# Optimization experiments

Hardware: AMD Instinct MI355X
Metric: run time of the kernel (lower is better)

## Reference

```python
import itertools
import jax, jax.numpy as jnp
import numpy as np

B, N, ETA, K, Z, HID, NATOM, NBOND = 128, 40, 64, 32, 32, 256, 24, 5
A = B * N
E = B * (N * (N - 1) // 2)
TAU = 1.0  # gumbel_softmax_temperature default


def _bn(x, g, b, eps=1e-5):
    # BatchNorm1d in training mode: batch statistics, biased variance
    m = jnp.mean(x, axis=0)
    v = jnp.var(x, axis=0)
    return (x - m) * jax.lax.rsqrt(v + eps) * g + b


def _prelu(x, a):
    return jnp.where(x >= 0, x, a * x)


def _mlp(x, w1, b1, g, be, a, w2, b2):
    # Linear -> BatchNorm1d -> PReLU -> Linear
    return _prelu(_bn(x @ w1 + b1, g, be), a) @ w2 + b2


def setup_inputs() -> dict:
    key = jax.random.key(0)
    ks = jax.random.split(key, 16)
    # static all-pairs edge index per graph, offset per graph (mirrors decode_z)
    pairs = np.array(list(itertools.combinations(range(N), 2)), dtype=np.int64)  # [P,2]
    offs = (np.arange(B, dtype=np.int64) * N)[:, None, None]
    edge_index = jnp.asarray((pairs[None] + offs).reshape(-1, 2))  # [E,2]
    node_graph_idx = jnp.asarray(np.repeat(np.arange(B, dtype=np.int64), N))  # [A]

    def w(k, shape, fan_in):
        return jax.random.normal(k, shape, jnp.float32) / np.sqrt(fan_in).astype(np.float32)

    return {
        "eta": jax.random.normal(ks[0], (B, ETA), jnp.float32),
        "gumbel_u": jax.random.uniform(ks[1], (A, K), jnp.float32, 1e-6, 1.0 - 1e-6),
        "noise_z": jax.random.normal(ks[2], (A, Z), jnp.float32),
        "edge_index": edge_index,
        "node_graph_idx": node_graph_idx,
        # cluster_mlp
        "cw1": w(ks[3], (ETA, HID), ETA), "cb1": jnp.zeros(HID), "cg": jnp.ones(HID), "cbe": jnp.zeros(HID), "ca": jnp.float32(0.25),
        "cw2": w(ks[4], (HID, K), HID), "cb2": jnp.zeros(K),
        # mixture params (torch: randn means, zero log-sigmas)
        "cm": jax.random.normal(ks[5], (K, Z), jnp.float32), "cls": jnp.zeros((K, Z), jnp.float32),
        # atom_classifier
        "aw1": w(ks[6], (Z, HID), Z), "ab1": jnp.zeros(HID), "ag": jnp.ones(HID), "abe": jnp.zeros(HID), "aa": jnp.float32(0.25),
        "aw2": w(ks[7], (HID, NATOM), HID), "ab2": jnp.zeros(NATOM),
        # bond bilinear tensor [d, a, b]
        "bm": jax.random.normal(ks[8], (Z, Z, Z), jnp.float32) / np.sqrt(Z).astype(np.float32),
        # bond_type_mlp
        "bw1": w(ks[9], (Z, HID), Z), "bb1": jnp.zeros(HID), "bg": jnp.ones(HID), "bbe": jnp.zeros(HID), "ba": jnp.float32(0.25),
        "bw2": w(ks[10], (HID, NBOND), HID), "bb2": jnp.zeros(NBOND),
    }


def reference(eta, gumbel_u, noise_z, edge_index, node_graph_idx,
              cw1, cb1, cg, cbe, ca, cw2, cb2, cm, cls,
              aw1, ab1, ag, abe, aa, aw2, ab2,
              bm, bw1, bb1, bg, bbe, ba, bw2, bb2):
    # decode_eta: pi = softmax(cluster_mlp(eta)); log_pi = log(pi)
    log_pi = jax.nn.log_softmax(_mlp(eta, cw1, cb1, cg, cbe, ca, cw2, cb2), axis=1)
    # repeat_interleave(log_pi, num_atoms) -> per-atom logits
    logits = log_pi[node_graph_idx]  # [A, K]
    # gumbel_softmax hard=True (straight-through)
    g = -jnp.log(-jnp.log(gumbel_u))
    y_soft = jax.nn.softmax((logits + g) / TAU, axis=1)
    y_hard = jax.nn.one_hot(jnp.argmax(y_soft, axis=1), K, dtype=y_soft.dtype)
    c = y_hard - jax.lax.stop_gradient(y_soft) + y_soft  # [A, K]
    # select cluster mean / log-sigma, reparameterize
    mu = c @ cm                 # [A, Z]
    log_sigma = c @ cls         # [A, Z]
    z = noise_z * jnp.exp(jnp.clip(log_sigma, -20.0, 30.0)) + mu
    # decode_z
    atom_types = _mlp(z, aw1, ab1, ag, abe, aa, aw2, ab2)  # [A, NATOM]
    Wm = 0.5 * (bm + jnp.swapaxes(bm, 1, 2))  # symmetrize over (a, b)
    zi = z[edge_index[:, 0]]  # [E, Z]
    zj = z[edge_index[:, 1]]  # [E, Z]
    t = jnp.einsum('ea,dab->edb', zi, Wm)       # [E, Z, Z]
    edge_feat = jnp.einsum('edb,eb->ed', t, zj)  # z_i^T W_d z_j, [E, Z]
    edge_types = jax.nn.softmax(_mlp(edge_feat, bw1, bb1, bg, bbe, ba, bw2, bb2), axis=1)  # [E, NBOND]
    return atom_types, edge_types
```

## Files before the change

### kernel.cpp

```cpp
#include <hip/hip_runtime.h>
#include <math.h>

#define BG    128
#define NN    40
#define AK    32
#define ZD    32
#define HIDN  256
#define ETAD  64
#define NATOM 24
#define NBOND 5
#define NA    (BG*NN)
#define EPG   (NN*(NN-1)/2)
#define NE    (BG*EPG)

typedef __attribute__((ext_vector_type(8))) short bf16x8;
typedef __attribute__((ext_vector_type(4))) float f32x4;

__device__ __forceinline__ unsigned short f2bf(float f) {
    union { float f; unsigned int u; } x; x.f = f;
    unsigned int r = x.u + 0x7fffu + ((x.u >> 16) & 1u);
    return (unsigned short)(r >> 16);
}
__device__ __forceinline__ unsigned int pk2bf(float lo, float hi) {
    return (unsigned int)f2bf(lo) | ((unsigned int)f2bf(hi) << 16);
}

__global__ __launch_bounds__(256) void k_pre(const float* __restrict__ bm,
                                             const float* __restrict__ bw1,
                                             const float* __restrict__ aw1,
                                             const float* __restrict__ aw2,
                                             const float* __restrict__ eta,
                                             const float* __restrict__ cw1,
                                             const float* __restrict__ cb1,
                                             unsigned short* __restrict__ wmpk,
                                             unsigned short* __restrict__ bpack,
                                             unsigned short* __restrict__ apk1,
                                             unsigned short* __restrict__ apk2,
                                             float* __restrict__ h1,
                                             float* __restrict__ cpart,
                                             float* __restrict__ zacc) {
    int b = blockIdx.x, t = threadIdx.x;
    if (b < 128) {
        int idx = b*256 + t;
        int d = idx >> 10;
        int Bt = (idx >> 9) & 1, ln = (idx >> 3) & 63, j = idx & 7;
        int al = Bt*16 + (ln & 15);
        int be = (ln >> 4)*8 + j;
        float v = 0.5f * (bm[d*1024 + al*32 + be] + bm[d*1024 + be*32 + al]);
        wmpk[idx] = f2bf(v);
    } else if (b < 160) {
        int idx = (b - 128)*256 + t;
        int ct = idx >> 9, rem = idx & 511;
        int lane = rem >> 3, j = rem & 7;
        bpack[idx] = f2bf(bw1[((lane >> 4)*8 + j)*HIDN + ct*16 + (lane & 15)]);
    } else if (b < 192) {
        int idx = (b - 160)*256 + t;
        int ct = idx >> 9, rem = idx & 511;
        int lane = rem >> 3, j = rem & 7;
        apk1[idx] = f2bf(aw1[((lane >> 4)*8 + j)*HIDN + ct*16 + (lane & 15)]);
    } else if (b < 224) {
        int idx = (b - 192)*256 + t;
        int f = idx >> 9, rem = idx & 511;
        int lane = rem >> 3, j = rem & 7;
        int kc = f >> 1, ot = f & 1;
        int col = ot*16 + (lane & 15);
        int k = kc*32 + (lane >> 4)*8 + j;
        apk2[idx] = (col < NATOM) ? f2bf(aw2[k*NATOM + col]) : 0;
    } else if (b < 232) {
        __shared__ float es[16*ETAD];
        int b2 = b - 224;
        int r0 = b2*16;
        for (int i = t; i < 16*ETAD; i += 256) es[i] = eta[r0*ETAD + i];
        __syncthreads();
        int c = t;
        float bias = cb1[c], s = 0.f, ss = 0.f;
        for (int r = 0; r < 16; ++r) {
            float acc = bias;
#pragma unroll
            for (int a = 0; a < ETAD; ++a) acc += es[r*ETAD + a] * cw1[a*HIDN + c];
            h1[(r0 + r)*HIDN + c] = acc;
            s += acc; ss += acc*acc;
        }
        cpart[b2*512 + c] = s;
        cpart[b2*512 + 256 + c] = ss;
    } else {
        for (int i = t; i < 2112; i += 256) zacc[i] = 0.f;
    }
}

__global__ __launch_bounds__(256) void k_edge_class(const float* __restrict__ h1,
                                                    const float* __restrict__ cpart,
                                                    const float* __restrict__ cg,
                                                    const float* __restrict__ cbe,
                                                    const float* __restrict__ ca,
                                                    const float* __restrict__ cw2,
                                                    const float* __restrict__ cb2,
                                                    const float* __restrict__ gum,
                                                    const float* __restrict__ noise,
                                                    const float* __restrict__ cm,
                                                    const float* __restrict__ cls,
                                                    const unsigned short* __restrict__ wmpk,
                                                    float* __restrict__ z,
                                                    float* __restrict__ mom_z,
                                                    float* __restrict__ ef) {
    __shared__ float zl[NN*36];
    __shared__ float p[HIDN];
    __shared__ float vp2[256];
    __shared__ float oo[AK];
    __shared__ float lp[AK];
    __shared__ unsigned short zfrag[3*512];
    __shared__ unsigned short Tf[4][3*512];
    __shared__ float efl[EPG*9];
    int t = threadIdx.x;
    int g = blockIdx.x >> 2, dg = blockIdx.x & 3;
    float aP = ca[0];

    {
        float s = 0.f, ss = 0.f;
#pragma unroll
        for (int q = 0; q < 8; ++q) { s += cpart[q*512 + t]; ss += cpart[q*512 + 256 + t]; }
        float m = s * (1.0f/(float)BG);
        float v = ss * (1.0f/(float)BG) - m*m;
        float x = h1[g*HIDN + t];
        float xn = (x - m) * (1.0f/sqrtf(v + 1e-5f)) * cg[t] + cbe[t];
        p[t] = xn >= 0.f ? xn : aP*xn;
    }
    __syncthreads();
    {
        int k = t & 31, part = t >> 5;
        float acc = 0.f;
        const float* pc = &p[part*32];
        const float* wc = &cw2[(part*32)*AK + k];
#pragma unroll
        for (int c = 0; c < 32; ++c) acc += pc[c] * wc[c*AK];
        vp2[t] = acc;
    }
    __syncthreads();
    if (t < AK) {
        float acc = cb2[t];
#pragma unroll
        for (int q = 0; q < 8; ++q) acc += vp2[q*32 + t];
        oo[t] = acc;
    }
    __syncthreads();
    if (t < AK) {
        float m = -INFINITY;
#pragma unroll
        for (int k = 0; k < AK; ++k) m = fmaxf(m, oo[k]);
        float S = 0.f;
#pragma unroll
        for (int k = 0; k < AK; ++k) S += expf(oo[k] - m);
        lp[t] = oo[t] - m - logf(S);
    }
    __syncthreads();
    {
        int lane = t & 31;
#pragma unroll
        for (int nb = 0; nb < 5; ++nb) {
            int node = nb*8 + (t >> 5);
            int n = g*NN + node;
            float u = gum[(size_t)n*AK + lane];
            float x = lp[lane] - logf(-logf(u));
            float m = x;
#pragma unroll
            for (int s = 1; s < 32; s <<= 1) m = fmaxf(m, __shfl_xor(m, s, 32));
            float e = expf(x - m);
            float S = e;
#pragma unroll
            for (int s = 1; s < 32; s <<= 1) S += __shfl_xor(S, s, 32);
            unsigned long long bal = __ballot(x == m);
            unsigned grp = (unsigned)(bal >> (t & 32));
            int am = __ffs(grp) - 1;
            float best = 1.0f / S;
            float cam = (1.0f - best) + best;
            float ls = cam * cls[am*ZD + lane];
            ls = fminf(fmaxf(ls, -20.0f), 30.0f);
            float zv = noise[(size_t)n*ZD + lane]*expf(ls) + cam*cm[am*ZD + lane];
            zl[node*36 + lane] = zv;
            if (dg == 0) z[(size_t)n*ZD + lane] = zv;
        }
    }
    __syncthreads();
    if (dg == 0) {
        int a = t >> 3, b4 = (t & 7) << 2;
        float ax = 0.f, ay = 0.f, az = 0.f, aw = 0.f;
        float mx = 0.f, my = 0.f, mz = 0.f, mw = 0.f;
        for (int r = 0; r < NN; ++r) {
            float  va = zl[r*36 + a];
            float4 vb = *(const float4*)&zl[r*36 + b4];
            ax += va*vb.x; ay += va*vb.y; az += va*vb.z; aw += va*vb.w;
            mx += vb.x;    my += vb.y;    mz += vb.z;    mw += vb.w;
        }
        atomicAdd(&mom_z[a*ZD + b4 + 0], ax);
        atomicAdd(&mom_z[a*ZD + b4 + 1], ay);
        atomicAdd(&mom_z[a*ZD + b4 + 2], az);
        atomicAdd(&mom_z[a*ZD + b4 + 3], aw);
        if (a == 0) {
            atomicAdd(&mom_z[ZD*ZD + b4 + 0], mx);
            atomicAdd(&mom_z[ZD*ZD + b4 + 1], my);
            atomicAdd(&mom_z[ZD*ZD + b4 + 2], mz);
            atomicAdd(&mom_z[ZD*ZD + b4 + 3], mw);
        }
    }
    if (t < 192) {
        int I = t >> 6, ln = t & 63;
        int row = I*16 + (ln & 15), c0 = (ln >> 4)*8;
        unsigned int pk[4] = {0u, 0u, 0u, 0u};
        if (row < NN) {
            float4 v0 = *(const float4*)&zl[row*36 + c0];
            float4 v1 = *(const float4*)&zl[row*36 + c0 + 4];
            pk[0] = pk2bf(v0.x, v0.y); pk[1] = pk2bf(v0.z, v0.w);
            pk[2] = pk2bf(v1.x, v1.y); pk[3] = pk2bf(v1.z, v1.w);
        }
        *(uint4*)&zfrag[(I*64 + ln)*8] = make_uint4(pk[0], pk[1], pk[2], pk[3]);
    }
    __syncthreads();

    int w = t >> 6, lane = t & 63;
    int l15 = lane & 15, gq = lane >> 4;
    f32x4 zero4 = {0.f, 0.f, 0.f, 0.f};

    bf16x8 zf[3];
#pragma unroll
    for (int I = 0; I < 3; ++I) zf[I] = *(const bf16x8*)&zfrag[I*512 + lane*8];

    for (int dk = 0; dk < 2; ++dk) {
        int dd = w*2 + dk;
        int d  = dg*8 + dd;
        bf16x8 wA[2];
        wA[0] = *(const bf16x8*)&wmpk[(d*2 + 0)*512 + lane*8];
        wA[1] = *(const bf16x8*)&wmpk[(d*2 + 1)*512 + lane*8];

        unsigned short* tw = &Tf[w][0];
        int gqp_lo = (gq >> 1);
        int jo     = (gq & 1)*4;
#pragma unroll
        for (int Bt = 0; Bt < 2; ++Bt) {
#pragma unroll
            for (int I = 0; I < 3; ++I) {
                f32x4 c = __builtin_amdgcn_mfma_f32_16x16x32_bf16(wA[Bt], zf[I], zero4, 0, 0, 0);
                int gqp = Bt*2 + gqp_lo;
                int pos = I*512 + gqp*128 + l15*8 + jo;
                unsigned int d0 = pk2bf(c[0], c[1]);
                unsigned int d1 = pk2bf(c[2], c[3]);
                *(uint2*)&tw[pos] = make_uint2(d0, d1);
            }
        }
        __syncthreads();

        bf16x8 tf[3];
#pragma unroll
        for (int J = 0; J < 3; ++J) tf[J] = *(const bf16x8*)&Tf[w][J*512 + lane*8];

#pragma unroll
        for (int I = 0; I < 3; ++I) {
#pragma unroll
            for (int J = I; J < 3; ++J) {
                f32x4 gacc = __builtin_amdgcn_mfma_f32_16x16x32_bf16(zf[I], tf[J], zero4, 0, 0, 0);
                int j = J*16 + l15;
                if (j < NN) {
#pragma unroll
                    for (int r = 0; r < 4; ++r) {
                        int i = I*16 + 4*gq + r;
                        if (i < j) {
                            int e = i*(79 - i)/2 + (j - i - 1);
                            efl[e*9 + dd] = gacc[r];
                        }
                    }
                }
            }
        }
        __syncthreads();
    }

    size_t gE = (size_t)g * EPG;
    for (int idx = t; idx < EPG*8; idx += 256) {
        int e = idx >> 3, dd = idx & 7;
        ef[(gE + e)*ZD + dg*8 + dd] = efl[e*9 + dd];
    }
}

#define MOMB 192
__global__ __launch_bounds__(256) void k_moment(const float* __restrict__ src,
                                                float* __restrict__ mom, int nchunks) {
    __shared__ float sm[ZD*ZD + ZD];
    int t = threadIdx.x;
    for (int i = t; i < ZD*ZD + ZD; i += 256) sm[i] = 0.f;
    __syncthreads();
    int lane = t & 63, wv = t >> 6;
    int l15 = lane & 15, g4 = lane >> 4;
    int wgid = blockIdx.x * 4 + wv;
    const int nw = MOMB * 4;
    f32x4 aII = {0,0,0,0}, aIJ = {0,0,0,0}, aJI = {0,0,0,0}, aJJ = {0,0,0,0};
    float mI = 0.f, mJ = 0.f;
    for (int ch = wgid; ch < nchunks; ch += nw) {
        const float* p = src + ((size_t)ch*32 + g4*8)*ZD + l15;
        float vI[8], vJ[8];
#pragma unroll
        for (int j = 0; j < 8; ++j) { vI[j] = p[j*ZD]; vJ[j] = p[j*ZD + 16]; }
        bf16x8 fI, fJ;
#pragma unroll
        for (int j = 0; j < 8; ++j) {
            fI[j] = (short)f2bf(vI[j]); fJ[j] = (short)f2bf(vJ[j]);
            mI += vI[j]; mJ += vJ[j];
        }
        aII = __builtin_amdgcn_mfma_f32_16x16x32_bf16(fI, fI, aII, 0, 0, 0);
        aIJ = __builtin_amdgcn_mfma_f32_16x16x32_bf16(fI, fJ, aIJ, 0, 0, 0);
        aJI = __builtin_amdgcn_mfma_f32_16x16x32_bf16(fJ, fI, aJI, 0, 0, 0);
        aJJ = __builtin_amdgcn_mfma_f32_16x16x32_bf16(fJ, fJ, aJJ, 0, 0, 0);
    }
#pragma unroll
    for (int r = 0; r < 4; ++r) {
        int row = g4*4 + r;
        atomicAdd(&sm[row*ZD + l15],             aII[r]);
        atomicAdd(&sm[row*ZD + 16 + l15],        aIJ[r]);
        atomicAdd(&sm[(16 + row)*ZD + l15],      aJI[r]);
        atomicAdd(&sm[(16 + row)*ZD + 16 + l15], aJJ[r]);
    }
    atomicAdd(&sm[ZD*ZD + l15], mI);
    atomicAdd(&sm[ZD*ZD + 16 + l15], mJ);
    __syncthreads();
    for (int i = t; i < ZD*ZD + ZD; i += 256) atomicAdd(&mom[i], sm[i]);
}

__global__ __launch_bounds__(256) void k_prep2(const float* __restrict__ mom_z,
                                               const float* __restrict__ mom_ef,
                                               const float* __restrict__ aw1,
                                               const float* __restrict__ ab1,
                                               const float* __restrict__ ag,
                                               const float* __restrict__ abe,
                                               const float* __restrict__ bw1,
                                               const float* __restrict__ bb1,
                                               const float* __restrict__ bg,
                                               const float* __restrict__ bbe,
                                               float* __restrict__ ascale,
                                               float* __restrict__ ashift,
                                               float* __restrict__ bscale,
                                               float* __restrict__ bshift) {
    bool bond = blockIdx.x >= 8;
    const float* mom = bond ? mom_ef : mom_z;
    const float* w1  = bond ? bw1 : aw1;
    const float* b1  = bond ? bb1 : ab1;
    const float* g   = bond ? bg  : ag;
    const float* be  = bond ? bbe : abe;
    float inv_n      = bond ? (1.0f/(float)NE) : (1.0f/(float)NA);
    float* scale     = bond ? bscale : ascale;
    float* shift     = bond ? bshift : ashift;

    __shared__ float mean[ZD];
    __shared__ float cov[ZD*ZD];
    __shared__ float vp[256], mp[256];
    int t = threadIdx.x;
    if (t < ZD) mean[t] = mom[ZD*ZD + t] * inv_n;
    __syncthreads();
    for (int pp = t; pp < ZD*ZD; pp += 256) {
        int a = pp >> 5, b = pp & 31;
        cov[pp] = mom[pp] * inv_n - mean[a]*mean[b];
    }
    __syncthreads();
    int c = (blockIdx.x & 7) * 32 + (t & 31);
    int part = t >> 5;
    float wr[ZD];
#pragma unroll
    for (int b = 0; b < ZD; ++b) wr[b] = w1[b*HIDN + c];
    float var = 0.f, mh = 0.f;
#pragma unroll
    for (int q = 0; q < 4; ++q) {
        int a = part*4 + q;
        float tmp = 0.f;
#pragma unroll
        for (int b = 0; b < ZD; ++b) tmp += cov[a*ZD + b] * wr[b];
        var += tmp * wr[a];
        mh  += mean[a] * wr[a];
    }
    vp[t] = var; mp[t] = mh;
    __syncthreads();
    if (t < 32) {
        float v = 0.f, m = 0.f;
#pragma unroll
        for (int q = 0; q < 8; ++q) { v += vp[q*32 + t]; m += mp[q*32 + t]; }
        m += b1[c];
        float rs = rsqrtf(fmaxf(v, 0.f) + 1e-5f) * g[c];
        scale[c] = rs;
        shift[c] = be[c] - m * rs;
    }
}

#define PSH 264
#define ATOMB (NA/64)
#define BROWS4 128
__global__ __launch_bounds__(256) void k_out(const float* __restrict__ z,
                                             const unsigned short* __restrict__ apk1,
                                             const unsigned short* __restrict__ apk2,
                                             const float* __restrict__ ab1,
                                             const float* __restrict__ ascale,
                                             const float* __restrict__ ashift,
                                             const float* __restrict__ aa,
                                             const float* __restrict__ ab2,
                                             const float* __restrict__ ef,
                                             const unsigned short* __restrict__ bpack,
                                             const float* __restrict__ bb1,
                                             const float* __restrict__ bscale,
                                             const float* __restrict__ bshift,
                                             const float* __restrict__ ba,
                                             const float* __restrict__ bw2,
                                             const float* __restrict__ bb2,
                                             float* __restrict__ out_atom,
                                             float* __restrict__ out_bond) {
    __shared__ unsigned short smu[4*16*PSH];
    int t = threadIdx.x;
    int w = t >> 6, lane = t & 63;
    int l15 = lane & 15, gq = lane >> 4;
    f32x4 zero4 = {0.f, 0.f, 0.f, 0.f};

    if (blockIdx.x < ATOMB) {
        size_t r0 = (size_t)blockIdx.x * 64 + (size_t)w * 16;
        float aP = aa[0];
        unsigned short* ptw = &smu[w*16*PSH];

        const float* zp = &z[(r0 + l15)*ZD + gq*8];
        float4 z0 = *(const float4*)zp;
        float4 z1 = *(const float4*)(zp + 4);
        bf16x8 af;
        af[0] = (short)f2bf(z0.x); af[1] = (short)f2bf(z0.y);
        af[2] = (short)f2bf(z0.z); af[3] = (short)f2bf(z0.w);
        af[4] = (short)f2bf(z1.x); af[5] = (short)f2bf(z1.y);
        af[6] = (short)f2bf(z1.z); af[7] = (short)f2bf(z1.w);

#pragma unroll
        for (int ct = 0; ct < 16; ++ct) {
            bf16x8 bf = *(const bf16x8*)&apk1[ct*512 + lane*8];
            f32x4 c = __builtin_amdgcn_mfma_f32_16x16x32_bf16(af, bf, zero4, 0, 0, 0);
            int ch = ct*16 + l15;
            float sc = ascale[ch];
            float sh = ashift[ch] + ab1[ch]*sc;
#pragma unroll
            for (int r = 0; r < 4; ++r) {
                float xn = c[r]*sc + sh;
                float pv = xn >= 0.f ? xn : aP*xn;
                ptw[(4*gq + r)*PSH + ch] = f2bf(pv);
            }
        }

        f32x4 o0 = zero4, o1 = zero4;
#pragma unroll
        for (int kc = 0; kc < 8; ++kc) {
            bf16x8 af2 = *(const bf16x8*)&ptw[l15*PSH + kc*32 + gq*8];
            bf16x8 b0 = *(const bf16x8*)&apk2[(kc*2 + 0)*512 + lane*8];
            bf16x8 b1 = *(const bf16x8*)&apk2[(kc*2 + 1)*512 + lane*8];
            o0 = __builtin_amdgcn_mfma_f32_16x16x32_bf16(af2, b0, o0, 0, 0, 0);
            o1 = __builtin_amdgcn_mfma_f32_16x16x32_bf16(af2, b1, o1, 0, 0, 0);
        }
#pragma unroll
        for (int r = 0; r < 4; ++r) {
            size_t row = r0 + 4*gq + r;
            out_atom[row*NATOM + l15] = o0[r] + ab2[l15];
            if (l15 < 8) out_atom[row*NATOM + 16 + l15] = o1[r] + ab2[16 + l15];
        }
        return;
    }

    float* w2s = (float*)smu;
    float* scs = w2s + HIDN*NBOND;
    float* shs = scs + HIDN;
    size_t r0 = (size_t)(blockIdx.x - ATOMB) * BROWS4;

    for (int i = t; i < HIDN*NBOND; i += 256) w2s[i] = bw2[i];
    { float sc = bscale[t]; scs[t] = sc; shs[t] = bshift[t] + bb1[t]*sc; }
    __syncthreads();

    float aP = ba[0];
    float b2r[NBOND];
#pragma unroll
    for (int k = 0; k < NBOND; ++k) b2r[k] = bb2[k];

#pragma unroll
    for (int rt = 0; rt < 2; ++rt) {
        size_t rowt = r0 + (size_t)(w*2 + rt)*16;
        const float* ar = &ef[(rowt + l15)*ZD + gq*8];
        float4 a0 = *(const float4*)ar;
        float4 a1 = *(const float4*)(ar + 4);
        bf16x8 af;
        af[0] = (short)f2bf(a0.x); af[1] = (short)f2bf(a0.y);
        af[2] = (short)f2bf(a0.z); af[3] = (short)f2bf(a0.w);
        af[4] = (short)f2bf(a1.x); af[5] = (short)f2bf(a1.y);
        af[6] = (short)f2bf(a1.z); af[7] = (short)f2bf(a1.w);

        float part[4][NBOND];
#pragma unroll
        for (int r = 0; r < 4; ++r)
#pragma unroll
            for (int k = 0; k < NBOND; ++k) part[r][k] = 0.f;

#pragma unroll
        for (int h = 0; h < 2; ++h) {
            bf16x8 bfr[8];
#pragma unroll
            for (int q = 0; q < 8; ++q)
                bfr[q] = *(const bf16x8*)&bpack[(h*8 + q)*512 + lane*8];
            f32x4 acc[8];
#pragma unroll
            for (int q = 0; q < 8; ++q)
                acc[q] = __builtin_amdgcn_mfma_f32_16x16x32_bf16(af, bfr[q], zero4, 0, 0, 0);
#pragma unroll
            for (int q = 0; q < 8; ++q) {
                int c = (h*8 + q)*16 + l15;
                float sc = scs[c], sh = shs[c];
                float w0 = w2s[c*NBOND+0], w1v = w2s[c*NBOND+1], w2v = w2s[c*NBOND+2];
                float w3 = w2s[c*NBOND+3], w4 = w2s[c*NBOND+4];
#pragma unroll
                for (int r = 0; r < 4; ++r) {
                    float xn = acc[q][r]*sc + sh;
                    float pv = xn >= 0.f ? xn : aP*xn;
                    part[r][0] += pv*w0; part[r][1] += pv*w1v; part[r][2] += pv*w2v;
                    part[r][3] += pv*w3; part[r][4] += pv*w4;
                }
            }
        }

#pragma unroll
        for (int s = 1; s < 16; s <<= 1) {
#pragma unroll
            for (int r = 0; r < 4; ++r)
#pragma unroll
                for (int k = 0; k < NBOND; ++k)
                    part[r][k] += __shfl_xor(part[r][k], s, 64);
        }

        if (l15 == 0) {
#pragma unroll
            for (int r = 0; r < 4; ++r) {
                size_t row = rowt + gq*4 + r;
                float lg[NBOND];
                float m = -INFINITY;
#pragma unroll
                for (int k = 0; k < NBOND; ++k) { lg[k] = part[r][k] + b2r[k]; m = fmaxf(m, lg[k]); }
                float S = 0.f;
#pragma unroll
                for (int k = 0; k < NBOND; ++k) { lg[k] = expf(lg[k] - m); S += lg[k]; }
                float invS = 1.f / S;
#pragma unroll
                for (int k = 0; k < NBOND; ++k) out_bond[row*NBOND + k] = lg[k] * invS;
            }
        }
    }
}

extern "C" void kernel_launch(void* const* d_in, const int* in_sizes, int n_in,
                              void* d_out, int out_size, void* d_ws, size_t ws_size,
                              hipStream_t stream) {
    (void)in_sizes; (void)n_in; (void)out_size; (void)ws_size;
    const float* eta  = (const float*)d_in[0];
    const float* gum  = (const float*)d_in[1];
    const float* noi  = (const float*)d_in[2];
    const float* cw1  = (const float*)d_in[5];
    const float* cb1  = (const float*)d_in[6];
    const float* cgp  = (const float*)d_in[7];
    const float* cbe  = (const float*)d_in[8];
    const float* ca   = (const float*)d_in[9];
    const float* cw2  = (const float*)d_in[10];
    const float* cb2  = (const float*)d_in[11];
    const float* cm   = (const float*)d_in[12];
    const float* cls  = (const float*)d_in[13];
    const float* aw1  = (const float*)d_in[14];
    const float* ab1  = (const float*)d_in[15];
    const float* ag   = (const float*)d_in[16];
    const float* abe  = (const float*)d_in[17];
    const float* aa   = (const float*)d_in[18];
    const float* aw2  = (const float*)d_in[19];
    const float* ab2  = (const float*)d_in[20];
    const float* bm   = (const float*)d_in[21];
    const float* bw1  = (const float*)d_in[22];
    const float* bb1  = (const float*)d_in[23];
    const float* bg   = (const float*)d_in[24];
    const float* bbe  = (const float*)d_in[25];
    const float* ba   = (const float*)d_in[26];
    const float* bw2  = (const float*)d_in[27];
    const float* bb2  = (const float*)d_in[28];
    float* out = (float*)d_out;
    float* ws  = (float*)d_ws;

    float*          mom_z  = ws;
    float*          mom_ef = ws + 1056;
    float*          ascale = ws + 2112;
    float*          ashift = ws + 2368;
    float*          bscale = ws + 2624;
    float*          bshift = ws + 2880;
    float*          cpart  = ws + 3136;
    unsigned short* bpack  = (unsigned short*)(ws + 7232);
    unsigned short* apk1   = (unsigned short*)(ws + 11328);
    unsigned short* apk2   = (unsigned short*)(ws + 15424);
    unsigned short* wmpk   = (unsigned short*)(ws + 19520);
    float*          h1     = ws + 35904;
    float*          zbuf   = ws + 68672;
    float*          efb    = ws + 232512;

    k_pre       <<<dim3(233),      dim3(256), 0, stream>>>(bm, bw1, aw1, aw2, eta, cw1, cb1,
                                                           wmpk, bpack, apk1, apk2, h1, cpart, ws);
    k_edge_class<<<dim3(4*BG),     dim3(256), 0, stream>>>(h1, cpart, cgp, cbe, ca, cw2, cb2,
                                                           gum, noi, cm, cls, wmpk,
                                                           zbuf, mom_z, efb);
    k_moment    <<<dim3(MOMB),     dim3(256), 0, stream>>>(efb, mom_ef, NE/32);
    k_prep2     <<<dim3(16),       dim3(256), 0, stream>>>(mom_z, mom_ef, aw1, ab1, ag, abe,
                                                           bw1, bb1, bg, bbe,
                                                           ascale, ashift, bscale, bshift);
    k_out       <<<dim3(ATOMB + NE/BROWS4), dim3(256), 0, stream>>>(
                                                           zbuf, apk1, apk2, ab1, ascale, ashift,
                                                           aa, ab2,
                                                           efb, bpack, bb1, bscale, bshift,
                                                           ba, bw2, bb2,
                                                           out, out + NA*NATOM);
}
```

Before: 81.17 us.

## Remove BN-prep kernel by fusing stats into moment and output kernels

Deletes the separate k_prep2 launch. The atom BatchNorm scale/shift is now computed by an extra block of k_moment, and every bond block of k_out recomputes the bond scale/shift from the edge moments in its prologue. The edge-feature buffer also moves to a dim-group-major layout ([4][NE][8]), so the edge-kernel stores and the moment/output loads become contiguous. This saves one launch and its dependency gap, at the cost of redundant per-block covariance work in the many k_out bond blocks. The bond bias bb1 is dropped from the shift, which is exact because the batch mean cancels it.

```diff
diff --git a/kernel.cpp b/kernel.cpp
--- a/kernel.cpp
+++ b/kernel.cpp
@@ -273,18 +273,60 @@
         __syncthreads();
     }
 
-    size_t gE = (size_t)g * EPG;
+    size_t base = ((size_t)dg*NE + (size_t)g*EPG)*8;
     for (int idx = t; idx < EPG*8; idx += 256) {
         int e = idx >> 3, dd = idx & 7;
-        ef[(gE + e)*ZD + dg*8 + dd] = efl[e*9 + dd];
+        ef[base + idx] = efl[e*9 + dd];
     }
 }
 
 #define MOMB 192
 __global__ __launch_bounds__(256) void k_moment(const float* __restrict__ src,
-                                                float* __restrict__ mom, int nchunks) {
+                                                float* __restrict__ mom,
+                                                const float* __restrict__ mom_z,
+                                                const float* __restrict__ aw1,
+                                                const float* __restrict__ ab1,
+                                                const float* __restrict__ ag,
+                                                const float* __restrict__ abe,
+                                                float* __restrict__ ascale,
+                                                float* __restrict__ ashift,
+                                                int nchunks) {
     __shared__ float sm[ZD*ZD + ZD];
     int t = threadIdx.x;
+
+    if (blockIdx.x == MOMB) {
+        float* cov = sm;
+        float* mean = sm + ZD*ZD;
+        if (t < ZD) mean[t] = mom_z[ZD*ZD + t] * (1.0f/(float)NA);
+        __syncthreads();
+        for (int pp = t; pp < ZD*ZD; pp += 256) {
+            int a = pp >> 5, b = pp & 31;
+            cov[pp] = mom_z[pp] * (1.0f/(float)NA) - mean[a]*mean[b];
+        }
+        __syncthreads();
+        int c = t;
+        float wr[ZD];
+#pragma unroll
+        for (int b = 0; b < ZD; ++b) wr[b] = aw1[b*HIDN + c];
+        float var = 0.f, mh = 0.f;
+        for (int a = 0; a < ZD; ++a) {
+            float tmp = 0.f;
+            const float4* cr = (const float4*)&cov[a*ZD];
+#pragma unroll
+            for (int b4 = 0; b4 < 8; ++b4) {
+                float4 cv = cr[b4];
+                tmp += cv.x*wr[b4*4] + cv.y*wr[b4*4+1] + cv.z*wr[b4*4+2] + cv.w*wr[b4*4+3];
+            }
+            var += tmp * wr[a];
+            mh  += mean[a] * wr[a];
+        }
+        mh += ab1[c];
+        float rs = rsqrtf(fmaxf(var, 0.f) + 1e-5f) * ag[c];
+        ascale[c] = rs;
+        ashift[c] = abe[c] - mh * rs;
+        return;
+    }
+
     for (int i = t; i < ZD*ZD + ZD; i += 256) sm[i] = 0.f;
     __syncthreads();
     int lane = t & 63, wv = t >> 6;
@@ -293,11 +335,14 @@
     const int nw = MOMB * 4;
     f32x4 aII = {0,0,0,0}, aIJ = {0,0,0,0}, aJI = {0,0,0,0}, aJJ = {0,0,0,0};
     float mI = 0.f, mJ = 0.f;
+    int segI = l15 >> 3, offI = l15 & 7;
     for (int ch = wgid; ch < nchunks; ch += nw) {
-        const float* p = src + ((size_t)ch*32 + g4*8)*ZD + l15;
+        size_t br = (size_t)ch*32 + g4*8;
+        const float* pI = src + ((size_t)segI*NE + br)*8 + offI;
+        const float* pJ = src + ((size_t)(2 + segI)*NE + br)*8 + offI;
         float vI[8], vJ[8];
 #pragma unroll
-        for (int j = 0; j < 8; ++j) { vI[j] = p[j*ZD]; vJ[j] = p[j*ZD + 16]; }
+        for (int j = 0; j < 8; ++j) { vI[j] = pI[j*8]; vJ[j] = pJ[j*8]; }
         bf16x8 fI, fJ;
 #pragma unroll
         for (int j = 0; j < 8; ++j) {
@@ -321,69 +366,6 @@
     atomicAdd(&sm[ZD*ZD + 16 + l15], mJ);
     __syncthreads();
     for (int i = t; i < ZD*ZD + ZD; i += 256) atomicAdd(&mom[i], sm[i]);
-}
-
-__global__ __launch_bounds__(256) void k_prep2(const float* __restrict__ mom_z,
-                                               const float* __restrict__ mom_ef,
-                                               const float* __restrict__ aw1,
-                                               const float* __restrict__ ab1,
-                                               const float* __restrict__ ag,
-                                               const float* __restrict__ abe,
-                                               const float* __restrict__ bw1,
-                                               const float* __restrict__ bb1,
-                                               const float* __restrict__ bg,
-                                               const float* __restrict__ bbe,
-                                               float* __restrict__ ascale,
-                                               float* __restrict__ ashift,
-                                               float* __restrict__ bscale,
-                                               float* __restrict__ bshift) {
-    bool bond = blockIdx.x >= 8;
-    const float* mom = bond ? mom_ef : mom_z;
-    const float* w1  = bond ? bw1 : aw1;
-    const float* b1  = bond ? bb1 : ab1;
-    const float* g   = bond ? bg  : ag;
-    const float* be  = bond ? bbe : abe;
-    float inv_n      = bond ? (1.0f/(float)NE) : (1.0f/(float)NA);
-    float* scale     = bond ? bscale : ascale;
-    float* shift     = bond ? bshift : ashift;
-
-    __shared__ float mean[ZD];
-    __shared__ float cov[ZD*ZD];
-    __shared__ float vp[256], mp[256];
-    int t = threadIdx.x;
-    if (t < ZD) mean[t] = mom[ZD*ZD + t] * inv_n;
-    __syncthreads();
-    for (int pp = t; pp < ZD*ZD; pp += 256) {
-        int a = pp >> 5, b = pp & 31;
-        cov[pp] = mom[pp] * inv_n - mean[a]*mean[b];
-    }
-    __syncthreads();
-    int c = (blockIdx.x & 7) * 32 + (t & 31);
-    int part = t >> 5;
-    float wr[ZD];
-#pragma unroll
-    for (int b = 0; b < ZD; ++b) wr[b] = w1[b*HIDN + c];
-    float var = 0.f, mh = 0.f;
-#pragma unroll
-    for (int q = 0; q < 4; ++q) {
-        int a = part*4 + q;
-        float tmp = 0.f;
-#pragma unroll
-        for (int b = 0; b < ZD; ++b) tmp += cov[a*ZD + b] * wr[b];
-        var += tmp * wr[a];
-        mh  += mean[a] * wr[a];
-    }
-    vp[t] = var; mp[t] = mh;
-    __syncthreads();
-    if (t < 32) {
-        float v = 0.f, m = 0.f;
-#pragma unroll
-        for (int q = 0; q < 8; ++q) { v += vp[q*32 + t]; m += mp[q*32 + t]; }
-        m += b1[c];
-        float rs = rsqrtf(fmaxf(v, 0.f) + 1e-5f) * g[c];
-        scale[c] = rs;
-        shift[c] = be[c] - m * rs;
-    }
 }
 
 #define PSH 264
@@ -399,9 +381,10 @@
                                              const float* __restrict__ ab2,
                                              const float* __restrict__ ef,
                                              const unsigned short* __restrict__ bpack,
-                                             const float* __restrict__ bb1,
-                                             const float* __restrict__ bscale,
-                                             const float* __restrict__ bshift,
+                                             const float* __restrict__ mom_ef,
+                                             const float* __restrict__ bw1,
+                                             const float* __restrict__ bg,
+                                             const float* __restrict__ bbe,
                                              const float* __restrict__ ba,
                                              const float* __restrict__ bw2,
                                              const float* __restrict__ bb2,
@@ -460,13 +443,42 @@
         return;
     }
 
-    float* w2s = (float*)smu;
-    float* scs = w2s + HIDN*NBOND;
-    float* shs = scs + HIDN;
+    float* w2s  = (float*)smu;
+    float* scs  = w2s + HIDN*NBOND;
+    float* shs  = scs + HIDN;
+    float* mean = shs + HIDN;
+    float* cov  = mean + 32;
     size_t r0 = (size_t)(blockIdx.x - ATOMB) * BROWS4;
 
     for (int i = t; i < HIDN*NBOND; i += 256) w2s[i] = bw2[i];
-    { float sc = bscale[t]; scs[t] = sc; shs[t] = bshift[t] + bb1[t]*sc; }
+    if (t < ZD) mean[t] = mom_ef[ZD*ZD + t] * (1.0f/(float)NE);
+    __syncthreads();
+    for (int pp = t; pp < ZD*ZD; pp += 256) {
+        int a = pp >> 5, bb = pp & 31;
+        cov[pp] = mom_ef[pp] * (1.0f/(float)NE) - mean[a]*mean[bb];
+    }
+    __syncthreads();
+    {
+        int c = t;
+        float wr[ZD];
+#pragma unroll
+        for (int bb = 0; bb < ZD; ++bb) wr[bb] = bw1[bb*HIDN + c];
+        float var = 0.f, mh = 0.f;
+        for (int a = 0; a < ZD; ++a) {
+            float tmp = 0.f;
+            const float4* cr = (const float4*)&cov[a*ZD];
+#pragma unroll
+            for (int b4 = 0; b4 < 8; ++b4) {
+                float4 cv = cr[b4];
+                tmp += cv.x*wr[b4*4] + cv.y*wr[b4*4+1] + cv.z*wr[b4*4+2] + cv.w*wr[b4*4+3];
+            }
+            var += tmp * wr[a];
+            mh  += mean[a] * wr[a];
+        }
+        float rs = rsqrtf(fmaxf(var, 0.f) + 1e-5f) * bg[c];
+        scs[c] = rs;
+        shs[c] = bbe[c] - mh * rs;
+    }
     __syncthreads();
 
     float aP = ba[0];
@@ -477,7 +489,7 @@
 #pragma unroll
     for (int rt = 0; rt < 2; ++rt) {
         size_t rowt = r0 + (size_t)(w*2 + rt)*16;
-        const float* ar = &ef[(rowt + l15)*ZD + gq*8];
+        const float* ar = &ef[((size_t)gq*NE + rowt + l15)*8];
         float4 a0 = *(const float4*)ar;
         float4 a1 = *(const float4*)(ar + 4);
         bf16x8 af;
@@ -577,6 +589,7 @@
     const float* ba   = (const float*)d_in[26];
     const float* bw2  = (const float*)d_in[27];
     const float* bb2  = (const float*)d_in[28];
+    (void)bb1;
     float* out = (float*)d_out;
     float* ws  = (float*)d_ws;
 
@@ -584,30 +597,27 @@
     float*          mom_ef = ws + 1056;
     float*          ascale = ws + 2112;
     float*          ashift = ws + 2368;
-    float*          bscale = ws + 2624;
-    float*          bshift = ws + 2880;
-    float*          cpart  = ws + 3136;
-    unsigned short* bpack  = (unsigned short*)(ws + 7232);
-    unsigned short* apk1   = (unsigned short*)(ws + 11328);
-    unsigned short* apk2   = (unsigned short*)(ws + 15424);
-    unsigned short* wmpk   = (unsigned short*)(ws + 19520);
-    float*          h1     = ws + 35904;
-    float*          zbuf   = ws + 68672;
-    float*          efb    = ws + 232512;
+    float*          cpart  = ws + 2624;
+    unsigned short* bpack  = (unsigned short*)(ws + 6720);
+    unsigned short* apk1   = (unsigned short*)(ws + 10816);
+    unsigned short* apk2   = (unsigned short*)(ws + 14912);
+    unsigned short* wmpk   = (unsigned short*)(ws + 19008);
+    float*          h1     = ws + 35392;
+    float*          zbuf   = ws + 68160;
+    float*          efb    = ws + 232000;
 
     k_pre       <<<dim3(233),      dim3(256), 0, stream>>>(bm, bw1, aw1, aw2, eta, cw1, cb1,
                                                            wmpk, bpack, apk1, apk2, h1, cpart, ws);
     k_edge_class<<<dim3(4*BG),     dim3(256), 0, stream>>>(h1, cpart, cgp, cbe, ca, cw2, cb2,
                                                            gum, noi, cm, cls, wmpk,
                                                            zbuf, mom_z, efb);
-    k_moment    <<<dim3(MOMB),     dim3(256), 0, stream>>>(efb, mom_ef, NE/32);
-    k_prep2     <<<dim3(16),       dim3(256), 0, stream>>>(mom_z, mom_ef, aw1, ab1, ag, abe,
-                                                           bw1, bb1, bg, bbe,
-                                                           ascale, ashift, bscale, bshift);
+    k_moment    <<<dim3(MOMB+1),   dim3(256), 0, stream>>>(efb, mom_ef, mom_z,
+                                                           aw1, ab1, ag, abe,
+                                                           ascale, ashift, NE/32);
     k_out       <<<dim3(ATOMB + NE/BROWS4), dim3(256), 0, stream>>>(
                                                            zbuf, apk1, apk2, ab1, ascale, ashift,
                                                            aa, ab2,
-                                                           efb, bpack, bb1, bscale, bshift,
+                                                           efb, bpack, mom_ef, bw1, bg, bbe,
                                                            ba, bw2, bb2,
                                                            out, out + NA*NATOM);
 }
```

New measurement: 91.76 us. 13.0% more time.
